# Kernel optimization log

Measured on AMD Instinct MI355X. Metric: run time of the kernel, lower is better.

Reference implementation:

```python
import jax, jax.numpy as jnp
import numpy as np

N = 50000          # num nodes
E = 800000         # num edges (avg degree 16)
IN_C, HID_C, OUT_C = 128, 128, 64
LPA_ITER = 5


def setup_inputs() -> dict:
    key = jax.random.key(0)
    ks = jax.random.split(key, 8)
    x = jax.random.normal(ks[0], (N, IN_C), dtype=jnp.float32)
    soft_labels = jax.random.uniform(ks[1], (N, OUT_C), dtype=jnp.float32)
    edge_index = jax.random.randint(ks[2], (2, E), 0, N, dtype=jnp.int64)
    # learnable edge weights: abs() in the original, so keep them positive
    edge_attr = jax.random.uniform(ks[3], (E,), dtype=jnp.float32, minval=0.1, maxval=1.0)
    # GCNConv params (lin weight + bias)
    w1 = jax.random.normal(ks[4], (IN_C, HID_C), dtype=jnp.float32) / np.sqrt(IN_C)
    b1 = jnp.zeros((HID_C,), dtype=jnp.float32)
    w2 = jax.random.normal(ks[5], (HID_C, OUT_C), dtype=jnp.float32) / np.sqrt(HID_C)
    b2 = jnp.zeros((OUT_C,), dtype=jnp.float32)
    return {"x": x, "soft_labels": soft_labels, "edge_attr": edge_attr,
            "w1": w1, "b1": b1, "w2": w2, "b2": b2, "edge_index": edge_index}


def reference(x, soft_labels, edge_attr, w1, b1, w2, b2, edge_index):
    row, col = edge_index[0], edge_index[1]
    n = x.shape[0]
    # row-normalize the weighted sparse adjacency: A_n = D^{-1} A
    deg = jax.ops.segment_sum(edge_attr, row, num_segments=n)  # [N]
    deg_inv = jnp.where(deg == 0, 0.0, 1.0 / deg)              # inf -> 0
    val = deg_inv[row] * edge_attr                              # [E]

    def spmm(v):  # A_n @ v,  v: [N, F]
        return jax.ops.segment_sum(val[:, None] * v[col], row, num_segments=n)

    # eval mode: dropout(p=0.5, training=False) is identity
    h = jax.nn.relu(spmm(x @ w1) + b1)        # GCNConv 1 (normalize=False)
    logits = spmm(h @ w2) + b2                # GCNConv 2
    x_out = jax.nn.sigmoid(logits)

    labels = soft_labels
    for _ in range(LPA_ITER):                 # label propagation
        labels = spmm(labels)
    labels = jax.nn.sigmoid(labels)
    return (x_out, labels)
```

## Files before the change

kernel.cpp:

```cpp
#include <hip/hip_runtime.h>
#include <cstdint>
#include <cstddef>


#define WS_ALIGN(x) (((x) + 255) & ~((size_t)255))

typedef __attribute__((ext_vector_type(8))) short short8;
typedef __attribute__((ext_vector_type(4))) float floatx4;

__device__ __forceinline__ unsigned short f2bf(float f) {
    unsigned u = __float_as_uint(f);
    u += 0x7fffu + ((u >> 16) & 1u);
    return (unsigned short)(u >> 16);
}
__device__ __forceinline__ float bf_lo(unsigned u) { return __uint_as_float(u << 16); }
__device__ __forceinline__ float bf_hi(unsigned u) { return __uint_as_float(u & 0xffff0000u); }
__device__ __forceinline__ unsigned pack_bf2(float a, float b) {
    return (unsigned)f2bf(a) | ((unsigned)f2bf(b) << 16);
}
__device__ __forceinline__ float sigmoidf(float x) {
    return 1.f / (1.f + __expf(-x));
}
__device__ __forceinline__ int2 ld_nt_int2(const int2* p) {
    long long v = __builtin_nontemporal_load((const long long*)p);
    int2 r;
    r.x = (int)(unsigned)(v & 0xffffffffLL);
    r.y = (int)(v >> 32);
    return r;
}

static const int NBLK = 256;
#define MAXNB 256

__device__ __forceinline__ void binA_count_body(const int* __restrict__ row,
                                                int* __restrict__ bucket_count,
                                                int* __restrict__ bases,
                                                int E, int chunk, int NB, int blk)
{
    __shared__ int hist[MAXNB];
    const int t = threadIdx.x;
    if (t < NB) hist[t] = 0;
    __syncthreads();
    const int s = blk * chunk;
    const int e = min(E, s + chunk);
    for (int i = s + t; i < e; i += 256)
        atomicAdd(&hist[row[i] >> 8], 1);
    __syncthreads();
    if (t < NB)
        bases[blk * NB + t] = atomicAdd(&bucket_count[t], hist[t]);
}

__launch_bounds__(256)
__global__ void bin_scan(const int* __restrict__ bucket_count, int* __restrict__ bucket_start,
                         int NB)
{
    __shared__ int s[256];
    const int t = threadIdx.x;
    int v = (t < NB) ? bucket_count[t] : 0;
    s[t] = v;
    __syncthreads();
    for (int off = 1; off < 256; off <<= 1) {
        int u = (t >= off) ? s[t - off] : 0;
        __syncthreads();
        s[t] += u;
        __syncthreads();
    }
    int excl = s[t] - v;
    if (t <= NB) bucket_start[t] = excl;
}

__device__ __forceinline__ void binA_scatter_body(const int* __restrict__ row,
                                                  const int* __restrict__ colv,
                                                  const float* __restrict__ ea,
                                                  const int* __restrict__ bucket_start,
                                                  const int* __restrict__ bases,
                                                  int2* __restrict__ bk,
                                                  int E, int chunk, int NB, int blk)
{
    __shared__ int cur[MAXNB];
    const int t = threadIdx.x;
    if (t < NB) cur[t] = bucket_start[t] + bases[blk * NB + t];
    __syncthreads();
    const int s = blk * chunk;
    const int e = min(E, s + chunk);
    for (int i = s + t; i < e; i += 256) {
        int r = row[i];
        int bin = r >> 8;
        int pos = atomicAdd(&cur[bin], 1);
        bk[pos] = make_int2(((r & 255) << 16) | colv[i], __float_as_int(ea[i]));
    }
}

__launch_bounds__(256)
__global__ void binB(const int2* __restrict__ bk, const int* __restrict__ bucket_start,
                     int* __restrict__ rowptr, int2* __restrict__ edges, int N)
{
    __shared__ int cnt[256];
    __shared__ float deg[256];
    __shared__ float inv[256];
    __shared__ int excl_s[256];
    __shared__ int cur[256];
    __shared__ int scantmp[256];
    const int b = blockIdx.x;
    const int t = threadIdx.x;
    const int s = bucket_start[b];
    const int e = bucket_start[b + 1];
    cnt[t] = 0;
    deg[t] = 0.f;
    __syncthreads();
    for (int i = s + t; i < e; i += 256) {
        int2 v = bk[i];
        int rl = ((unsigned)v.x) >> 16;
        atomicAdd(&cnt[rl], 1);
        atomicAdd(&deg[rl], __int_as_float(v.y));
    }
    __syncthreads();
    const int myc = cnt[t];
    scantmp[t] = myc;
    __syncthreads();
    for (int off = 1; off < 256; off <<= 1) {
        int u = (t >= off) ? scantmp[t - off] : 0;
        __syncthreads();
        scantmp[t] += u;
        __syncthreads();
    }
    const int excl = scantmp[t] - myc;
    excl_s[t] = excl;
    float d = deg[t];
    inv[t] = (d > 0.f) ? 1.f / d : 0.f;
    cur[t] = 0;
    const int gr = b * 256 + t;
    if (gr <= N) rowptr[gr] = s + excl;
    __syncthreads();
    for (int i = s + t; i < e; i += 256) {
        int2 v = bk[i];
        int rl = ((unsigned)v.x) >> 16;
        int c = v.x & 0xffff;
        int p = s + excl_s[rl] + atomicAdd(&cur[rl], 1);
        edges[p] = make_int2(c, __float_as_int(__int_as_float(v.y) * inv[rl]));
    }
}

template<int COLS>
__device__ __forceinline__ void pack_w_body(const float* __restrict__ W,
                                            unsigned short* __restrict__ Wp, int idx)
{
    const int total = (COLS / 16) * 4 * 64;
    if (idx >= total) return;
    const int l = idx & 63;
    const int t = (idx >> 6) & 3;
    const int ct = idx >> 8;
    const int kbase = t * 32 + (l >> 4) * 8;
    const int col = ct * 16 + (l & 15);
    unsigned short v[8];
#pragma unroll
    for (int j = 0; j < 8; ++j)
        v[j] = f2bf(W[(size_t)(kbase + j) * COLS + col]);
    uint4 o;
    o.x = (unsigned)v[0] | ((unsigned)v[1] << 16);
    o.y = (unsigned)v[2] | ((unsigned)v[3] << 16);
    o.z = (unsigned)v[4] | ((unsigned)v[5] << 16);
    o.w = (unsigned)v[6] | ((unsigned)v[7] << 16);
    *(uint4*)(Wp + (size_t)idx * 8) = o;
}

__launch_bounds__(256)
__global__ void count_prep(const int* __restrict__ row, int* __restrict__ bucket_count,
                           int* __restrict__ bases, int E, int chunk, int NB,
                           const float* __restrict__ soft, unsigned short* __restrict__ softb,
                           int ns2,
                           const float* __restrict__ w1, unsigned short* __restrict__ w1p,
                           const float* __restrict__ w2, unsigned short* __restrict__ w2p)
{
    const int b = blockIdx.x;
    const int t = threadIdx.x;
    if (b < NBLK) {
        binA_count_body(row, bucket_count, bases, E, chunk, NB, b);
    } else {
        const int bb = b - NBLK;
        if (bb < 8) {
            pack_w_body<128>(w1, w1p, bb * 256 + t);
        } else if (bb < 12) {
            pack_w_body<64>(w2, w2p, (bb - 8) * 256 + t);
        } else {
            int i = (bb - 12) * 256 + t;
            if (i < ns2) {
                float2 v = ((const float2*)soft)[i];
                ((unsigned*)softb)[i] = pack_bf2(v.x, v.y);
            }
        }
    }
}

__device__ __forceinline__ void gemm128_f32a_body(const float* __restrict__ A,
                                                  const unsigned short* __restrict__ Wp,
                                                  unsigned short* __restrict__ C, int M, int bid)
{
    const int COLS = 128;
    const int wave = threadIdx.x >> 6;
    const int lane = threadIdx.x & 63;
    const int row0 = bid * 64 + wave * 16;
    const int m = lane & 15;
    const int q = lane >> 4;

    const int arow = row0 + m;
    const bool avalid = arow < M;
    short8 a[4];
#pragma unroll
    for (int t = 0; t < 4; ++t) {
        if (avalid) {
            float4 f0 = *(const float4*)(A + (size_t)arow * 128 + t * 32 + q * 8);
            float4 f1 = *(const float4*)(A + (size_t)arow * 128 + t * 32 + q * 8 + 4);
            a[t][0] = (short)f2bf(f0.x); a[t][1] = (short)f2bf(f0.y);
            a[t][2] = (short)f2bf(f0.z); a[t][3] = (short)f2bf(f0.w);
            a[t][4] = (short)f2bf(f1.x); a[t][5] = (short)f2bf(f1.y);
            a[t][6] = (short)f2bf(f1.z); a[t][7] = (short)f2bf(f1.w);
        } else {
            a[t] = (short8)0;
        }
    }

#pragma unroll
    for (int ct = 0; ct < COLS / 16; ++ct) {
        floatx4 acc = {0.f, 0.f, 0.f, 0.f};
#pragma unroll
        for (int t = 0; t < 4; ++t) {
            short8 b = *(const short8*)(Wp + (size_t)((ct * 4 + t) * 64 + lane) * 8);
            acc = __builtin_amdgcn_mfma_f32_16x16x32_bf16(a[t], b, acc, 0, 0, 0);
        }
        const int col = ct * 16 + m;
#pragma unroll
        for (int r = 0; r < 4; ++r) {
            int orow = row0 + q * 4 + r;
            if (orow < M)
                C[(size_t)orow * COLS + col] = f2bf(acc[r]);
        }
    }
}

__launch_bounds__(256)
__global__ void gemm_scatter(const float* __restrict__ A, const unsigned short* __restrict__ Wp,
                             unsigned short* __restrict__ C, int M, int gGemm,
                             const int* __restrict__ row, const int* __restrict__ colv,
                             const float* __restrict__ ea,
                             const int* __restrict__ bucket_start, const int* __restrict__ bases,
                             int2* __restrict__ bk, int E, int chunk, int NB)
{
    const int b = blockIdx.x;
    if (b < gGemm) {
        gemm128_f32a_body(A, Wp, C, M, b);
    } else {
        binA_scatter_body(row, colv, ea, bucket_start, bases, bk, E, chunk, NB, b - gGemm);
    }
}

template<int COLS>
__launch_bounds__(256)
__global__ void gemm_mfma(const unsigned short* __restrict__ A,
                          const unsigned short* __restrict__ Wp,
                          unsigned short* __restrict__ C, int M)
{
    const int wave = threadIdx.x >> 6;
    const int lane = threadIdx.x & 63;
    const int row0 = blockIdx.x * 64 + wave * 16;
    const int m = lane & 15;
    const int q = lane >> 4;

    const int arow = row0 + m;
    const bool avalid = arow < M;
    short8 a[4];
#pragma unroll
    for (int t = 0; t < 4; ++t) {
        if (avalid)
            a[t] = *(const short8*)(A + (size_t)arow * 128 + t * 32 + q * 8);
        else
            a[t] = (short8)0;
    }

#pragma unroll
    for (int ct = 0; ct < COLS / 16; ++ct) {
        floatx4 acc = {0.f, 0.f, 0.f, 0.f};
#pragma unroll
        for (int t = 0; t < 4; ++t) {
            short8 b = *(const short8*)(Wp + (size_t)((ct * 4 + t) * 64 + lane) * 8);
            acc = __builtin_amdgcn_mfma_f32_16x16x32_bf16(a[t], b, acc, 0, 0, 0);
        }
        const int col = ct * 16 + m;
#pragma unroll
        for (int r = 0; r < 4; ++r) {
            int orow = row0 + q * 4 + r;
            if (orow < M)
                C[(size_t)orow * COLS + col] = f2bf(acc[r]);
        }
    }
}

__launch_bounds__(256)
__global__ void fused1_pair(const int* __restrict__ rowptr, const int2* __restrict__ edges,
                            const uint2* __restrict__ srcA,
                            const unsigned* __restrict__ srcB,
                            const float* __restrict__ bias,
                            uint2* __restrict__ outA,
                            unsigned* __restrict__ outB,
                            int n)
{
    const int row = blockIdx.x * 4 + (threadIdx.x >> 6);
    const int lane = threadIdx.x & 63;
    const int f = lane & 31;
    const int half = lane >> 5;
    if (row >= n) return;
    const int s = rowptr[row];
    const int e = rowptr[row + 1];

    float a0[4], a1[4], b0[2], b1[2];
#pragma unroll
    for (int j = 0; j < 4; ++j) { a0[j] = 0.f; a1[j] = 0.f; }
    b0[0] = b0[1] = b1[0] = b1[1] = 0.f;

    int i = s;
    for (; i + 8 <= e; i += 8) {
        int2 ed[4]; uint2 ua[4]; unsigned ub[4];
#pragma unroll
        for (int j = 0; j < 4; ++j) ed[j] = ld_nt_int2(&edges[i + 2 * j + half]);
#pragma unroll
        for (int j = 0; j < 4; ++j) ua[j] = srcA[(size_t)ed[j].x * 32 + f];
#pragma unroll
        for (int j = 0; j < 4; ++j) ub[j] = srcB[(size_t)ed[j].x * 32 + f];
#pragma unroll
        for (int j = 0; j < 4; ++j) {
            float w = __int_as_float(ed[j].y);
            float* A = (j & 1) ? a1 : a0;
            float* B = (j & 1) ? b1 : b0;
            A[0] = fmaf(w, bf_lo(ua[j].x), A[0]);
            A[1] = fmaf(w, bf_hi(ua[j].x), A[1]);
            A[2] = fmaf(w, bf_lo(ua[j].y), A[2]);
            A[3] = fmaf(w, bf_hi(ua[j].y), A[3]);
            B[0] = fmaf(w, bf_lo(ub[j]), B[0]);
            B[1] = fmaf(w, bf_hi(ub[j]), B[1]);
        }
    }
    for (; i + 2 <= e; i += 2) {
        int2 ed = ld_nt_int2(&edges[i + half]);
        float w = __int_as_float(ed.y);
        uint2 ua = srcA[(size_t)ed.x * 32 + f];
        unsigned ub = srcB[(size_t)ed.x * 32 + f];
        a0[0] = fmaf(w, bf_lo(ua.x), a0[0]);
        a0[1] = fmaf(w, bf_hi(ua.x), a0[1]);
        a0[2] = fmaf(w, bf_lo(ua.y), a0[2]);
        a0[3] = fmaf(w, bf_hi(ua.y), a0[3]);
        b0[0] = fmaf(w, bf_lo(ub), b0[0]);
        b0[1] = fmaf(w, bf_hi(ub), b0[1]);
    }
    if (i < e && half == 0) {
        int2 ed = ld_nt_int2(&edges[i]);
        float w = __int_as_float(ed.y);
        uint2 ua = srcA[(size_t)ed.x * 32 + f];
        unsigned ub = srcB[(size_t)ed.x * 32 + f];
        a1[0] = fmaf(w, bf_lo(ua.x), a1[0]);
        a1[1] = fmaf(w, bf_hi(ua.x), a1[1]);
        a1[2] = fmaf(w, bf_lo(ua.y), a1[2]);
        a1[3] = fmaf(w, bf_hi(ua.y), a1[3]);
        b1[0] = fmaf(w, bf_lo(ub), b1[0]);
        b1[1] = fmaf(w, bf_hi(ub), b1[1]);
    }
    float A0 = a0[0] + a1[0], A1 = a0[1] + a1[1];
    float A2 = a0[2] + a1[2], A3 = a0[3] + a1[3];
    float B0 = b0[0] + b1[0], B1 = b0[1] + b1[1];
    A0 += __shfl_down(A0, 32); A1 += __shfl_down(A1, 32);
    A2 += __shfl_down(A2, 32); A3 += __shfl_down(A3, 32);
    B0 += __shfl_down(B0, 32); B1 += __shfl_down(B1, 32);
    if (half == 0) {
        float4 bb = *(const float4*)(bias + 4 * f);
        A0 = fmaxf(A0 + bb.x, 0.f);
        A1 = fmaxf(A1 + bb.y, 0.f);
        A2 = fmaxf(A2 + bb.z, 0.f);
        A3 = fmaxf(A3 + bb.w, 0.f);
        uint2 o;
        o.x = pack_bf2(A0, A1);
        o.y = pack_bf2(A2, A3);
        outA[(size_t)row * 32 + f] = o;
        outB[(size_t)row * 32 + f] = pack_bf2(B0, B1);
    }
}

__launch_bounds__(256)
__global__ void fused2_pair(const int* __restrict__ rowptr, const int2* __restrict__ edges,
                            const unsigned* __restrict__ srcA,
                            const unsigned* __restrict__ srcB,
                            const float* __restrict__ bias,
                            float* __restrict__ outA,
                            unsigned* __restrict__ outB,
                            int n)
{
    const int row = blockIdx.x * 4 + (threadIdx.x >> 6);
    const int lane = threadIdx.x & 63;
    const int f = lane & 31;
    const int half = lane >> 5;
    if (row >= n) return;
    const int s = rowptr[row];
    const int e = rowptr[row + 1];

    float a0[2], a1[2], b0[2], b1[2];
    a0[0] = a0[1] = a1[0] = a1[1] = 0.f;
    b0[0] = b0[1] = b1[0] = b1[1] = 0.f;

    int i = s;
    for (; i + 8 <= e; i += 8) {
        int2 ed[4]; unsigned ua[4], ub[4];
#pragma unroll
        for (int j = 0; j < 4; ++j) ed[j] = ld_nt_int2(&edges[i + 2 * j + half]);
#pragma unroll
        for (int j = 0; j < 4; ++j) ua[j] = srcA[(size_t)ed[j].x * 32 + f];
#pragma unroll
        for (int j = 0; j < 4; ++j) ub[j] = srcB[(size_t)ed[j].x * 32 + f];
#pragma unroll
        for (int j = 0; j < 4; ++j) {
            float w = __int_as_float(ed[j].y);
            float* A = (j & 1) ? a1 : a0;
            float* B = (j & 1) ? b1 : b0;
            A[0] = fmaf(w, bf_lo(ua[j]), A[0]);
            A[1] = fmaf(w, bf_hi(ua[j]), A[1]);
            B[0] = fmaf(w, bf_lo(ub[j]), B[0]);
            B[1] = fmaf(w, bf_hi(ub[j]), B[1]);
        }
    }
    for (; i + 2 <= e; i += 2) {
        int2 ed = ld_nt_int2(&edges[i + half]);
        float w = __int_as_float(ed.y);
        unsigned ua = srcA[(size_t)ed.x * 32 + f];
        unsigned ub = srcB[(size_t)ed.x * 32 + f];
        a0[0] = fmaf(w, bf_lo(ua), a0[0]);
        a0[1] = fmaf(w, bf_hi(ua), a0[1]);
        b0[0] = fmaf(w, bf_lo(ub), b0[0]);
        b0[1] = fmaf(w, bf_hi(ub), b0[1]);
    }
    if (i < e && half == 0) {
        int2 ed = ld_nt_int2(&edges[i]);
        float w = __int_as_float(ed.y);
        unsigned ua = srcA[(size_t)ed.x * 32 + f];
        unsigned ub = srcB[(size_t)ed.x * 32 + f];
        a1[0] = fmaf(w, bf_lo(ua), a1[0]);
        a1[1] = fmaf(w, bf_hi(ua), a1[1]);
        b1[0] = fmaf(w, bf_lo(ub), b1[0]);
        b1[1] = fmaf(w, bf_hi(ub), b1[1]);
    }
    float A0 = a0[0] + a1[0], A1 = a0[1] + a1[1];
    float B0 = b0[0] + b1[0], B1 = b0[1] + b1[1];
    A0 += __shfl_down(A0, 32); A1 += __shfl_down(A1, 32);
    B0 += __shfl_down(B0, 32); B1 += __shfl_down(B1, 32);
    if (half == 0) {
        float2 bb = *(const float2*)(bias + 2 * f);
        float2 o;
        o.x = sigmoidf(A0 + bb.x);
        o.y = sigmoidf(A1 + bb.y);
        *(float2*)(outA + (size_t)row * 64 + 2 * f) = o;
        outB[(size_t)row * 32 + f] = pack_bf2(B0, B1);
    }
}

template<int ACT>
__launch_bounds__(256)
__global__ void spmm64_pair(const int* __restrict__ rowptr, const int2* __restrict__ edges,
                            const unsigned* __restrict__ src,
                            void* __restrict__ out, int n)
{
    const int row = blockIdx.x * 4 + (threadIdx.x >> 6);
    const int lane = threadIdx.x & 63;
    const int f = lane & 31;
    const int half = lane >> 5;
    if (row >= n) return;
    const int s = rowptr[row];
    const int e = rowptr[row + 1];

    float a[4][2];
#pragma unroll
    for (int j = 0; j < 4; ++j) { a[j][0] = 0.f; a[j][1] = 0.f; }

    int i = s;
    for (; i + 8 <= e; i += 8) {
        int2 ed[4]; unsigned u[4];
#pragma unroll
        for (int j = 0; j < 4; ++j) ed[j] = ld_nt_int2(&edges[i + 2 * j + half]);
#pragma unroll
        for (int j = 0; j < 4; ++j) u[j] = src[(size_t)ed[j].x * 32 + f];
#pragma unroll
        for (int j = 0; j < 4; ++j) {
            float w = __int_as_float(ed[j].y);
            a[j][0] = fmaf(w, bf_lo(u[j]), a[j][0]);
            a[j][1] = fmaf(w, bf_hi(u[j]), a[j][1]);
        }
    }
    for (; i + 2 <= e; i += 2) {
        int2 ed = ld_nt_int2(&edges[i + half]);
        float w = __int_as_float(ed.y);
        unsigned u = src[(size_t)ed.x * 32 + f];
        a[0][0] = fmaf(w, bf_lo(u), a[0][0]);
        a[0][1] = fmaf(w, bf_hi(u), a[0][1]);
    }
    if (i < e && half == 0) {
        int2 ed = ld_nt_int2(&edges[i]);
        float w = __int_as_float(ed.y);
        unsigned u = src[(size_t)ed.x * 32 + f];
        a[1][0] = fmaf(w, bf_lo(u), a[1][0]);
        a[1][1] = fmaf(w, bf_hi(u), a[1][1]);
    }
    float v0 = (a[0][0] + a[1][0]) + (a[2][0] + a[3][0]);
    float v1 = (a[0][1] + a[1][1]) + (a[2][1] + a[3][1]);
    v0 += __shfl_down(v0, 32);
    v1 += __shfl_down(v1, 32);
    if (half == 0) {
        if (ACT == 0) {
            ((unsigned*)out)[(size_t)row * 32 + f] = pack_bf2(v0, v1);
        } else {
            float2 o;
            o.x = sigmoidf(v0);
            o.y = sigmoidf(v1);
            *(float2*)((float*)out + (size_t)row * 64 + 2 * f) = o;
        }
    }
}

extern "C" void kernel_launch(void* const* d_in, const int* in_sizes, int n_in,
                              void* d_out, int out_size, void* d_ws, size_t ws_size,
                              hipStream_t stream)
{
    const float* x    = (const float*)d_in[0];
    const float* soft = (const float*)d_in[1];
    const float* ea   = (const float*)d_in[2];
    const float* w1   = (const float*)d_in[3];
    const float* b1   = (const float*)d_in[4];
    const float* w2   = (const float*)d_in[5];
    const float* b2   = (const float*)d_in[6];
    const int*   eidx = (const int*)d_in[7];

    const int N = in_sizes[0] / 128;
    const int E = in_sizes[2];
    const int* row  = eidx;
    const int* colv = eidx + E;
    const int NB = (N + 255) / 256;
    const int chunk = (E + NBLK - 1) / NBLK;

    uint8_t* ws = (uint8_t*)d_ws;
    size_t off = 0;
    auto alloc = [&](size_t bytes) -> void* {
        void* p = ws + off;
        off += WS_ALIGN(bytes);
        return p;
    };
    int*  bucket_count = (int*) alloc((size_t)NB * 4);
    int*  bucket_start = (int*) alloc(((size_t)NB + 1) * 4);
    int*  bases        = (int*) alloc((size_t)NBLK * NB * 4);
    int*  rowptr       = (int*) alloc(((size_t)N + 1) * 4);
    int2* bk           = (int2*)alloc((size_t)E * 8);
    int2* edges        = (int2*)alloc((size_t)E * 8 + 64);
    unsigned short* w1p     = (unsigned short*)alloc((size_t)128 * 128 * 2);
    unsigned short* w2p     = (unsigned short*)alloc((size_t)128 * 64 * 2);
    unsigned short* xw1b    = (unsigned short*)alloc((size_t)N * 128 * 2);
    unsigned short* hb      = (unsigned short*)alloc((size_t)N * 128 * 2);
    unsigned short* logitsb = (unsigned short*)alloc((size_t)N * 64 * 2);
    unsigned short* softb   = (unsigned short*)alloc((size_t)N * 64 * 2);
    unsigned short* labA    = (unsigned short*)alloc((size_t)N * 64 * 2);
    unsigned short* labB    = (unsigned short*)alloc((size_t)N * 64 * 2);

    float* out0 = (float*)d_out;
    float* out1 = out0 + (size_t)N * 64;

    hipMemsetAsync(bucket_count, 0, (size_t)NB * 4, stream);

    const int ns2 = (N * 64) / 2;
    const int gGemm = (N + 63) / 64;
    const int gSp   = (N + 3) / 4;

    const int gCP = NBLK + 12 + (ns2 + 255) / 256;
    count_prep<<<gCP, 256, 0, stream>>>(row, bucket_count, bases, E, chunk, NB,
                                        soft, softb, ns2, w1, w1p, w2, w2p);

    bin_scan<<<1, 256, 0, stream>>>(bucket_count, bucket_start, NB);

    gemm_scatter<<<gGemm + NBLK, 256, 0, stream>>>(x, w1p, xw1b, N, gGemm,
                                                   row, colv, ea, bucket_start, bases,
                                                   bk, E, chunk, NB);

    binB<<<NB, 256, 0, stream>>>(bk, bucket_start, rowptr, edges, N);

    fused1_pair<<<gSp, 256, 0, stream>>>(rowptr, edges, (const uint2*)xw1b,
                                         (const unsigned*)softb, b1,
                                         (uint2*)hb, (unsigned*)labA, N);

    gemm_mfma<64><<<gGemm, 256, 0, stream>>>(hb, w2p, logitsb, N);

    fused2_pair<<<gSp, 256, 0, stream>>>(rowptr, edges, (const unsigned*)logitsb,
                                         (const unsigned*)labA, b2,
                                         out0, (unsigned*)labB, N);

    spmm64_pair<0><<<gSp, 256, 0, stream>>>(rowptr, edges, (const unsigned*)labB, labA, N);
    spmm64_pair<0><<<gSp, 256, 0, stream>>>(rowptr, edges, (const unsigned*)labA, labB, N);
    spmm64_pair<3><<<gSp, 256, 0, stream>>>(rowptr, edges, (const unsigned*)labB, out1, N);
}
```

Before: 306.9 us.

## Fold bucket scan into count kernel and co-launch layer-2 GEMM with label SpMM

The single-block bucket scan now runs inside count_prep: the last block to finish, found through an atomic counter, computes the exclusive scan, so one launch disappears. The second GEMM (h @ w2) is merged into one launch with the second label-propagation SpMM, since the two are independent. The label-propagation iterations are reordered around fused2_pair so the total number of launches drops. This trades launch gaps and tail idling for an extra atomic and threadfence and heavier mixed blocks in one grid.

```diff
diff --git a/kernel.cpp b/kernel.cpp
--- a/kernel.cpp
+++ b/kernel.cpp
@@ -48,25 +48,6 @@
     __syncthreads();
     if (t < NB)
         bases[blk * NB + t] = atomicAdd(&bucket_count[t], hist[t]);
-}
-
-__launch_bounds__(256)
-__global__ void bin_scan(const int* __restrict__ bucket_count, int* __restrict__ bucket_start,
-                         int NB)
-{
-    __shared__ int s[256];
-    const int t = threadIdx.x;
-    int v = (t < NB) ? bucket_count[t] : 0;
-    s[t] = v;
-    __syncthreads();
-    for (int off = 1; off < 256; off <<= 1) {
-        int u = (t >= off) ? s[t - off] : 0;
-        __syncthreads();
-        s[t] += u;
-        __syncthreads();
-    }
-    int excl = s[t] - v;
-    if (t <= NB) bucket_start[t] = excl;
 }
 
 __device__ __forceinline__ void binA_scatter_body(const int* __restrict__ row,
@@ -166,7 +147,8 @@
 
 __launch_bounds__(256)
 __global__ void count_prep(const int* __restrict__ row, int* __restrict__ bucket_count,
-                           int* __restrict__ bases, int E, int chunk, int NB,
+                           int* __restrict__ bases, int* __restrict__ bucket_start,
+                           int E, int chunk, int NB,
                            const float* __restrict__ soft, unsigned short* __restrict__ softb,
                            int ns2,
                            const float* __restrict__ w1, unsigned short* __restrict__ w1p,
@@ -176,6 +158,25 @@
     const int t = threadIdx.x;
     if (b < NBLK) {
         binA_count_body(row, bucket_count, bases, E, chunk, NB, b);
+        __threadfence();
+        __shared__ int amLast;
+        if (t == 0)
+            amLast = (atomicAdd(&bucket_count[MAXNB], 1) == NBLK - 1);
+        __syncthreads();
+        if (amLast) {
+            __threadfence();
+            __shared__ int s[256];
+            int v = (t < NB) ? atomicAdd(&bucket_count[t], 0) : 0;
+            s[t] = v;
+            __syncthreads();
+            for (int off = 1; off < 256; off <<= 1) {
+                int u = (t >= off) ? s[t - off] : 0;
+                __syncthreads();
+                s[t] += u;
+                __syncthreads();
+            }
+            if (t <= NB) bucket_start[t] = s[t] - v;
+        }
     } else {
         const int bb = b - NBLK;
         if (bb < 8) {
@@ -238,6 +239,46 @@
     }
 }
 
+__device__ __forceinline__ void gemm64_body(const unsigned short* __restrict__ A,
+                                            const unsigned short* __restrict__ Wp,
+                                            unsigned short* __restrict__ C, int M, int bid)
+{
+    const int COLS = 64;
+    const int wave = threadIdx.x >> 6;
+    const int lane = threadIdx.x & 63;
+    const int row0 = bid * 64 + wave * 16;
+    const int m = lane & 15;
+    const int q = lane >> 4;
+
+    const int arow = row0 + m;
+    const bool avalid = arow < M;
+    short8 a[4];
+#pragma unroll
+    for (int t = 0; t < 4; ++t) {
+        if (avalid)
+            a[t] = *(const short8*)(A + (size_t)arow * 128 + t * 32 + q * 8);
+        else
+            a[t] = (short8)0;
+    }
+
+#pragma unroll
+    for (int ct = 0; ct < COLS / 16; ++ct) {
+        floatx4 acc = {0.f, 0.f, 0.f, 0.f};
+#pragma unroll
+        for (int t = 0; t < 4; ++t) {
+            short8 b = *(const short8*)(Wp + (size_t)((ct * 4 + t) * 64 + lane) * 8);
+            acc = __builtin_amdgcn_mfma_f32_16x16x32_bf16(a[t], b, acc, 0, 0, 0);
+        }
+        const int col = ct * 16 + m;
+#pragma unroll
+        for (int r = 0; r < 4; ++r) {
+            int orow = row0 + q * 4 + r;
+            if (orow < M)
+                C[(size_t)orow * COLS + col] = f2bf(acc[r]);
+        }
+    }
+}
+
 __launch_bounds__(256)
 __global__ void gemm_scatter(const float* __restrict__ A, const unsigned short* __restrict__ Wp,
                              unsigned short* __restrict__ C, int M, int gGemm,
@@ -254,44 +295,88 @@
     }
 }
 
-template<int COLS>
+template<int ACT>
+__device__ __forceinline__ void spmm64_body(const int* __restrict__ rowptr,
+                                            const int2* __restrict__ edges,
+                                            const unsigned* __restrict__ src,
+                                            void* __restrict__ out, int n, int bid)
+{
+    const int row = bid * 4 + (threadIdx.x >> 6);
+    const int lane = threadIdx.x & 63;
+    const int f = lane & 31;
+    const int half = lane >> 5;
+    if (row >= n) return;
+    const int s = rowptr[row];
+    const int e = rowptr[row + 1];
+
+    float a[4][2];
+#pragma unroll
+    for (int j = 0; j < 4; ++j) { a[j][0] = 0.f; a[j][1] = 0.f; }
+
+    int i = s;
+    for (; i + 8 <= e; i += 8) {
+        int2 ed[4]; unsigned u[4];
+#pragma unroll
+        for (int j = 0; j < 4; ++j) ed[j] = ld_nt_int2(&edges[i + 2 * j + half]);
+#pragma unroll
+        for (int j = 0; j < 4; ++j) u[j] = src[(size_t)ed[j].x * 32 + f];
+#pragma unroll
+        for (int j = 0; j < 4; ++j) {
+            float w = __int_as_float(ed[j].y);
+            a[j][0] = fmaf(w, bf_lo(u[j]), a[j][0]);
+            a[j][1] = fmaf(w, bf_hi(u[j]), a[j][1]);
+        }
+    }
+    for (; i + 2 <= e; i += 2) {
+        int2 ed = ld_nt_int2(&edges[i + half]);
+        float w = __int_as_float(ed.y);
+        unsigned u = src[(size_t)ed.x * 32 + f];
+        a[0][0] = fmaf(w, bf_lo(u), a[0][0]);
+        a[0][1] = fmaf(w, bf_hi(u), a[0][1]);
+    }
+    if (i < e && half == 0) {
+        int2 ed = ld_nt_int2(&edges[i]);
+        float w = __int_as_float(ed.y);
+        unsigned u = src[(size_t)ed.x * 32 + f];
+        a[1][0] = fmaf(w, bf_lo(u), a[1][0]);
+        a[1][1] = fmaf(w, bf_hi(u), a[1][1]);
+    }
+    float v0 = (a[0][0] + a[1][0]) + (a[2][0] + a[3][0]);
+    float v1 = (a[0][1] + a[1][1]) + (a[2][1] + a[3][1]);
+    v0 += __shfl_down(v0, 32);
+    v1 += __shfl_down(v1, 32);
+    if (half == 0) {
+        if (ACT == 0) {
+            ((unsigned*)out)[(size_t)row * 32 + f] = pack_bf2(v0, v1);
+        } else {
+            float2 o;
+            o.x = sigmoidf(v0);
+            o.y = sigmoidf(v1);
+            *(float2*)((float*)out + (size_t)row * 64 + 2 * f) = o;
+        }
+    }
+}
+
+template<int ACT>
 __launch_bounds__(256)
-__global__ void gemm_mfma(const unsigned short* __restrict__ A,
-                          const unsigned short* __restrict__ Wp,
-                          unsigned short* __restrict__ C, int M)
-{
-    const int wave = threadIdx.x >> 6;
-    const int lane = threadIdx.x & 63;
-    const int row0 = blockIdx.x * 64 + wave * 16;
-    const int m = lane & 15;
-    const int q = lane >> 4;
-
-    const int arow = row0 + m;
-    const bool avalid = arow < M;
-    short8 a[4];
-#pragma unroll
-    for (int t = 0; t < 4; ++t) {
-        if (avalid)
-            a[t] = *(const short8*)(A + (size_t)arow * 128 + t * 32 + q * 8);
-        else
-            a[t] = (short8)0;
-    }
-
-#pragma unroll
-    for (int ct = 0; ct < COLS / 16; ++ct) {
-        floatx4 acc = {0.f, 0.f, 0.f, 0.f};
-#pragma unroll
-        for (int t = 0; t < 4; ++t) {
-            short8 b = *(const short8*)(Wp + (size_t)((ct * 4 + t) * 64 + lane) * 8);
-            acc = __builtin_amdgcn_mfma_f32_16x16x32_bf16(a[t], b, acc, 0, 0, 0);
-        }
-        const int col = ct * 16 + m;
-#pragma unroll
-        for (int r = 0; r < 4; ++r) {
-            int orow = row0 + q * 4 + r;
-            if (orow < M)
-                C[(size_t)orow * COLS + col] = f2bf(acc[r]);
-        }
+__global__ void spmm64_pair(const int* __restrict__ rowptr, const int2* __restrict__ edges,
+                            const unsigned* __restrict__ src, void* __restrict__ out, int n)
+{
+    spmm64_body<ACT>(rowptr, edges, src, out, n, blockIdx.x);
+}
+
+__launch_bounds__(256)
+__global__ void gemm64_spmm(const unsigned short* __restrict__ A,
+                            const unsigned short* __restrict__ Wp,
+                            unsigned short* __restrict__ C, int M, int gGemm,
+                            const int* __restrict__ rowptr, const int2* __restrict__ edges,
+                            const unsigned* __restrict__ src, void* __restrict__ out, int n)
+{
+    const int b = blockIdx.x;
+    if (b < gGemm) {
+        gemm64_body(A, Wp, C, M, b);
+    } else {
+        spmm64_body<0>(rowptr, edges, src, out, n, b - gGemm);
     }
 }
 
@@ -458,68 +543,6 @@
     }
 }
 
-template<int ACT>
-__launch_bounds__(256)
-__global__ void spmm64_pair(const int* __restrict__ rowptr, const int2* __restrict__ edges,
-                            const unsigned* __restrict__ src,
-                            void* __restrict__ out, int n)
-{
-    const int row = blockIdx.x * 4 + (threadIdx.x >> 6);
-    const int lane = threadIdx.x & 63;
-    const int f = lane & 31;
-    const int half = lane >> 5;
-    if (row >= n) return;
-    const int s = rowptr[row];
-    const int e = rowptr[row + 1];
-
-    float a[4][2];
-#pragma unroll
-    for (int j = 0; j < 4; ++j) { a[j][0] = 0.f; a[j][1] = 0.f; }
-
-    int i = s;
-    for (; i + 8 <= e; i += 8) {
-        int2 ed[4]; unsigned u[4];
-#pragma unroll
-        for (int j = 0; j < 4; ++j) ed[j] = ld_nt_int2(&edges[i + 2 * j + half]);
-#pragma unroll
-        for (int j = 0; j < 4; ++j) u[j] = src[(size_t)ed[j].x * 32 + f];
-#pragma unroll
-        for (int j = 0; j < 4; ++j) {
-            float w = __int_as_float(ed[j].y);
-            a[j][0] = fmaf(w, bf_lo(u[j]), a[j][0]);
-            a[j][1] = fmaf(w, bf_hi(u[j]), a[j][1]);
-        }
-    }
-    for (; i + 2 <= e; i += 2) {
-        int2 ed = ld_nt_int2(&edges[i + half]);
-        float w = __int_as_float(ed.y);
-        unsigned u = src[(size_t)ed.x * 32 + f];
-        a[0][0] = fmaf(w, bf_lo(u), a[0][0]);
-        a[0][1] = fmaf(w, bf_hi(u), a[0][1]);
-    }
-    if (i < e && half == 0) {
-        int2 ed = ld_nt_int2(&edges[i]);
-        float w = __int_as_float(ed.y);
-        unsigned u = src[(size_t)ed.x * 32 + f];
-        a[1][0] = fmaf(w, bf_lo(u), a[1][0]);
-        a[1][1] = fmaf(w, bf_hi(u), a[1][1]);
-    }
-    float v0 = (a[0][0] + a[1][0]) + (a[2][0] + a[3][0]);
-    float v1 = (a[0][1] + a[1][1]) + (a[2][1] + a[3][1]);
-    v0 += __shfl_down(v0, 32);
-    v1 += __shfl_down(v1, 32);
-    if (half == 0) {
-        if (ACT == 0) {
-            ((unsigned*)out)[(size_t)row * 32 + f] = pack_bf2(v0, v1);
-        } else {
-            float2 o;
-            o.x = sigmoidf(v0);
-            o.y = sigmoidf(v1);
-            *(float2*)((float*)out + (size_t)row * 64 + 2 * f) = o;
-        }
-    }
-}
-
 extern "C" void kernel_launch(void* const* d_in, const int* in_sizes, int n_in,
                               void* d_out, int out_size, void* d_ws, size_t ws_size,
                               hipStream_t stream)
@@ -547,7 +570,7 @@
         off += WS_ALIGN(bytes);
         return p;
     };
-    int*  bucket_count = (int*) alloc((size_t)NB * 4);
+    int*  bucket_count = (int*) alloc(((size_t)MAXNB + 1) * 4);
     int*  bucket_start = (int*) alloc(((size_t)NB + 1) * 4);
     int*  bases        = (int*) alloc((size_t)NBLK * NB * 4);
     int*  rowptr       = (int*) alloc(((size_t)N + 1) * 4);
@@ -565,17 +588,15 @@
     float* out0 = (float*)d_out;
     float* out1 = out0 + (size_t)N * 64;
 
-    hipMemsetAsync(bucket_count, 0, (size_t)NB * 4, stream);
+    hipMemsetAsync(bucket_count, 0, ((size_t)MAXNB + 1) * 4, stream);
 
     const int ns2 = (N * 64) / 2;
     const int gGemm = (N + 63) / 64;
     const int gSp   = (N + 3) / 4;
 
     const int gCP = NBLK + 12 + (ns2 + 255) / 256;
-    count_prep<<<gCP, 256, 0, stream>>>(row, bucket_count, bases, E, chunk, NB,
-                                        soft, softb, ns2, w1, w1p, w2, w2p);
-
-    bin_scan<<<1, 256, 0, stream>>>(bucket_count, bucket_start, NB);
+    count_prep<<<gCP, 256, 0, stream>>>(row, bucket_count, bases, bucket_start,
+                                        E, chunk, NB, soft, softb, ns2, w1, w1p, w2, w2p);
 
     gemm_scatter<<<gGemm + NBLK, 256, 0, stream>>>(x, w1p, xw1b, N, gGemm,
                                                    row, colv, ea, bucket_start, bases,
@@ -587,13 +608,14 @@
                                          (const unsigned*)softb, b1,
                                          (uint2*)hb, (unsigned*)labA, N);
 
-    gemm_mfma<64><<<gGemm, 256, 0, stream>>>(hb, w2p, logitsb, N);
+    gemm64_spmm<<<gGemm + gSp, 256, 0, stream>>>(hb, w2p, logitsb, N, gGemm,
+                                                 rowptr, edges, (const unsigned*)labA,
+                                                 labB, N);
 
     fused2_pair<<<gSp, 256, 0, stream>>>(rowptr, edges, (const unsigned*)logitsb,
-                                         (const unsigned*)labA, b2,
-                                         out0, (unsigned*)labB, N);
-
-    spmm64_pair<0><<<gSp, 256, 0, stream>>>(rowptr, edges, (const unsigned*)labB, labA, N);
+                                         (const unsigned*)labB, b2,
+                                         out0, (unsigned*)labA, N);
+
     spmm64_pair<0><<<gSp, 256, 0, stream>>>(rowptr, edges, (const unsigned*)labA, labB, N);
     spmm64_pair<3><<<gSp, 256, 0, stream>>>(rowptr, edges, (const unsigned*)labB, out1, N);
 }
```

New measurement: 319.2 us. 1.04x slower.
